# Kernel optimization log

Measured on AMD Instinct MI355X. Metric: run time of the kernel, lower is better.

Reference implementation:

```python
import jax, jax.numpy as jnp
import numpy as np

NUM_NODES = 128
BATCH = 32768
G_BASE = np.array([8.0, 8.0, 16.0, 8.0, 8.0, 4.0, 8.0, 8.0, 4.0, 4.0, 4.0, 8.0], dtype=np.float32)
T_BASE = np.array([0.02, 0.02, 0.16, 0.28], dtype=np.float32)


def setup_inputs() -> dict:
    key = jax.random.key(0)
    k1, k2, k3, k4, k5, k6 = jax.random.split(key, 6)
    x = jax.random.normal(k1, (BATCH, NUM_NODES * 8), dtype=jnp.float32)
    t = jnp.zeros((), dtype=jnp.float32)
    node_connectivity = jax.random.normal(k2, (NUM_NODES, NUM_NODES), dtype=jnp.float32) * 0.1
    # per-node gain/time-constant params (init values + small perturbation so grads are generic)
    G = jnp.asarray(G_BASE)[None, :] * (1.0 + 0.05 * jax.random.normal(k3, (NUM_NODES, 12), dtype=jnp.float32))
    T = jnp.asarray(T_BASE)[None, :] * (1.0 + 0.05 * jax.random.normal(k4, (NUM_NODES, 4), dtype=jnp.float32))
    adaptation = jnp.ones((NUM_NODES,), dtype=jnp.float32) + 0.1 * jax.random.normal(k5, (NUM_NODES,), dtype=jnp.float32)
    R = jnp.ones((NUM_NODES,), dtype=jnp.float32) + 0.1 * jax.random.normal(k6, (NUM_NODES,), dtype=jnp.float32)
    return {"t": t, "x": x, "node_connectivity": node_connectivity, "G": G, "T": T,
            "adaptation": adaptation, "R": R}


def reference(t, x, node_connectivity, G, T, adaptation, R):
    # x: [B, N*8] state; activation = sigmoid branch of FlexibleCMC
    B = x.shape[0]
    N = node_connectivity.shape[0]
    x = jnp.clip(x, -100.0, 100.0)
    xs = x.reshape(B, N, 8)  # [B, N, 8]
    # S = sigmoid(R*x) - sigmoid(0)  (sigmoid activation branch)
    S = jax.nn.sigmoid(R[None, :, None] * xs) - 0.5  # [B, N, 8]
    # message passing: mean activity of each node, weighted by connectivity (no self-loop)
    m = xs.mean(axis=-1)  # [B, N]
    C = node_connectivity * (1.0 - jnp.eye(N, dtype=node_connectivity.dtype))
    node_input = jnp.einsum('bj,ij->bi', m, C)  # [B, N]
    scale = jax.nn.sigmoid(adaptation) * 0.1  # [N]

    g = lambda k: G[:, k]  # [N], broadcasts against [B, N]
    u1 = -g(0) * S[..., 0] - g(2) * S[..., 4] - g(1) * S[..., 2] + node_input
    f1 = scale * (u1 - 2.0 * xs[..., 1] - xs[..., 0] / T[:, 0]) / T[:, 0]
    u3 = g(7) * S[..., 0] - g(6) * S[..., 2] - g(11) * S[..., 4] + node_input
    f3 = scale * (u3 - 2.0 * xs[..., 3] - xs[..., 2] / T[:, 1]) / T[:, 1]
    u5 = g(4) * S[..., 0] + g(5) * S[..., 6] - g(3) * S[..., 4] + g(10) * S[..., 2] + node_input
    f5 = scale * (u5 - 2.0 * xs[..., 5] - xs[..., 4] / T[:, 2]) / T[:, 2]
    u7 = -g(9) * S[..., 6] - g(8) * S[..., 4] + node_input
    f7 = scale * (u7 - 2.0 * xs[..., 7] - xs[..., 6] / T[:, 3]) / T[:, 3]
    f0 = scale * xs[..., 1]
    f2 = scale * xs[..., 3]
    f4 = scale * xs[..., 5]
    f6 = scale * xs[..., 7]
    f = jnp.stack([f0, f1, f2, f3, f4, f5, f6, f7], axis=-1)  # [B, N, 8]
    return f.reshape(B, N * 8)
```

## Files before the change

kernel.cpp:

```cpp
#include <hip/hip_runtime.h>

#define NNODES 128
#define BATCH  32768
#define BLOCK  256
#define ROWS_PER_CHUNK 8
#define NCHUNKS (BATCH / ROWS_PER_CHUNK)
#define GRID   1024

__device__ __forceinline__ float sigmoidf_(float z) {
    return 1.0f / (1.0f + __expf(-z));
}

__device__ __forceinline__ float clipf_(float v) {
    return fminf(fmaxf(v, -100.0f), 100.0f);
}

__device__ __forceinline__ unsigned short bf16_(float f) {
    unsigned u = __float_as_uint(f);
    return (unsigned short)((u + 0x8000u) >> 16);
}

__device__ __forceinline__ void node_update(const float* xs8, float ni,
                                            const float* gi, const float* invTi,
                                            float sci, float Ri, float* f8) {
    float S0 = sigmoidf_(Ri * xs8[0]) - 0.5f;
    float S2 = sigmoidf_(Ri * xs8[2]) - 0.5f;
    float S4 = sigmoidf_(Ri * xs8[4]) - 0.5f;
    float S6 = sigmoidf_(Ri * xs8[6]) - 0.5f;
    float u1 = ni - gi[0] * S0 - gi[1] * S2 - gi[2]  * S4;
    float u3 = ni + gi[7] * S0 - gi[6] * S2 - gi[11] * S4;
    float u5 = ni + gi[4] * S0 + gi[10] * S2 - gi[3] * S4 + gi[5] * S6;
    float u7 = ni - gi[8] * S4 - gi[9] * S6;
    f8[0] = sci * xs8[1];
    f8[1] = sci * (u1 - 2.0f * xs8[1] - xs8[0] * invTi[0]) * invTi[0];
    f8[2] = sci * xs8[3];
    f8[3] = sci * (u3 - 2.0f * xs8[3] - xs8[2] * invTi[1]) * invTi[1];
    f8[4] = sci * xs8[5];
    f8[5] = sci * (u5 - 2.0f * xs8[5] - xs8[4] * invTi[2]) * invTi[2];
    f8[6] = sci * xs8[7];
    f8[7] = sci * (u7 - 2.0f * xs8[7] - xs8[6] * invTi[3]) * invTi[3];
}

__global__ __launch_bounds__(BLOCK, 2)
void cmc_kernel(const float* __restrict__ x,
                const float* __restrict__ C,
                const float* __restrict__ G,
                const float* __restrict__ T,
                const float* __restrict__ adap,
                const float* __restrict__ R,
                float* __restrict__ out)
{
    __shared__ uint4 ct4[32 * 64];
    __shared__ float m_lds[4][2][NNODES];

    const int tid  = threadIdx.x;
    const int lane = tid & 63;
    const int w    = tid >> 6;
    const int nA   = 2 * lane;

    {
        const int j0 = (tid & 31) * 4;
        const int j4 = j0 >> 2;
        const int tb = tid >> 5;
        #pragma unroll
        for (int it = 0; it < 4; ++it) {
            const int i0 = (tb + it * 8) * 4;
            float4 row[4];
            #pragma unroll
            for (int r = 0; r < 4; ++r)
                row[r] = *reinterpret_cast<const float4*>(C + (size_t)(i0 + r) * NNODES + j0);
            unsigned short t[4][4];
            #pragma unroll
            for (int r = 0; r < 4; ++r) {
                #pragma unroll
                for (int jj = 0; jj < 4; ++jj)
                    t[r][jj] = (i0 + r == j0 + jj) ? (unsigned short)0
                                                   : bf16_((&row[r].x)[jj]);
            }
            uint4 rec0, rec1;
            rec0.x = (unsigned)t[0][0] | ((unsigned)t[0][1] << 16);
            rec0.y = (unsigned)t[0][2] | ((unsigned)t[0][3] << 16);
            rec0.z = (unsigned)t[1][0] | ((unsigned)t[1][1] << 16);
            rec0.w = (unsigned)t[1][2] | ((unsigned)t[1][3] << 16);
            rec1.x = (unsigned)t[2][0] | ((unsigned)t[2][1] << 16);
            rec1.y = (unsigned)t[2][2] | ((unsigned)t[2][3] << 16);
            rec1.z = (unsigned)t[3][0] | ((unsigned)t[3][1] << 16);
            rec1.w = (unsigned)t[3][2] | ((unsigned)t[3][3] << 16);
            const int p0 = i0 >> 1;
            ct4[j4 * 64 + (p0 ^ j4)]       = rec0;
            ct4[j4 * 64 + ((p0 + 1) ^ j4)] = rec1;
        }
    }

    float g[2][12], invT[2][4], sc[2], Rr[2];
    #pragma unroll
    for (int i = 0; i < 2; ++i) {
        int n = nA + i;
        #pragma unroll
        for (int k = 0; k < 12; ++k) g[i][k] = G[n * 12 + k];
        #pragma unroll
        for (int k = 0; k < 4; ++k) invT[i][k] = 1.0f / T[n * 4 + k];
        sc[i] = 0.1f * sigmoidf_(adap[n]);
        Rr[i] = R[n];
    }

    __syncthreads();

    for (int chunk = blockIdx.x; chunk < NCHUNKS; chunk += GRID) {
        const int r0 = chunk * ROWS_PER_CHUNK + 2 * w;

        float xv[2][16];
        {
            const float4* p0 = reinterpret_cast<const float4*>(x + (size_t)r0 * 1024 + lane * 16);
            const float4* p1 = reinterpret_cast<const float4*>(x + (size_t)(r0 + 1) * 1024 + lane * 16);
            #pragma unroll
            for (int q = 0; q < 4; ++q) {
                float4 v = p0[q];
                xv[0][q * 4 + 0] = clipf_(v.x); xv[0][q * 4 + 1] = clipf_(v.y);
                xv[0][q * 4 + 2] = clipf_(v.z); xv[0][q * 4 + 3] = clipf_(v.w);
            }
            #pragma unroll
            for (int q = 0; q < 4; ++q) {
                float4 v = p1[q];
                xv[1][q * 4 + 0] = clipf_(v.x); xv[1][q * 4 + 1] = clipf_(v.y);
                xv[1][q * 4 + 2] = clipf_(v.z); xv[1][q * 4 + 3] = clipf_(v.w);
            }
        }

        #pragma unroll
        for (int rr = 0; rr < 2; ++rr) {
            float s0 = 0.0f, s1 = 0.0f;
            #pragma unroll
            for (int k = 0; k < 8; ++k) { s0 += xv[rr][k]; s1 += xv[rr][8 + k]; }
            float2 mv = make_float2(s0 * 0.125f, s1 * 0.125f);
            *reinterpret_cast<float2*>(&m_lds[w][rr][nA]) = mv;
        }

        float acc00 = 0.f, acc01 = 0.f, acc10 = 0.f, acc11 = 0.f;
        #pragma unroll 4
        for (int j4 = 0; j4 < 32; ++j4) {
            float4 mA = *reinterpret_cast<const float4*>(&m_lds[w][0][j4 * 4]);
            float4 mB = *reinterpret_cast<const float4*>(&m_lds[w][1][j4 * 4]);
            uint4 cu = ct4[j4 * 64 + (lane ^ j4)];
            float ce0 = __uint_as_float(cu.x << 16);
            float ce1 = __uint_as_float(cu.x & 0xffff0000u);
            float ce2 = __uint_as_float(cu.y << 16);
            float ce3 = __uint_as_float(cu.y & 0xffff0000u);
            float co0 = __uint_as_float(cu.z << 16);
            float co1 = __uint_as_float(cu.z & 0xffff0000u);
            float co2 = __uint_as_float(cu.w << 16);
            float co3 = __uint_as_float(cu.w & 0xffff0000u);
            acc00 = fmaf(mA.x, ce0, acc00); acc00 = fmaf(mA.y, ce1, acc00);
            acc00 = fmaf(mA.z, ce2, acc00); acc00 = fmaf(mA.w, ce3, acc00);
            acc01 = fmaf(mA.x, co0, acc01); acc01 = fmaf(mA.y, co1, acc01);
            acc01 = fmaf(mA.z, co2, acc01); acc01 = fmaf(mA.w, co3, acc01);
            acc10 = fmaf(mB.x, ce0, acc10); acc10 = fmaf(mB.y, ce1, acc10);
            acc10 = fmaf(mB.z, ce2, acc10); acc10 = fmaf(mB.w, ce3, acc10);
            acc11 = fmaf(mB.x, co0, acc11); acc11 = fmaf(mB.y, co1, acc11);
            acc11 = fmaf(mB.z, co2, acc11); acc11 = fmaf(mB.w, co3, acc11);
        }

        {
            float* o0 = out + (size_t)r0 * 1024 + lane * 16;
            float* o1 = out + (size_t)(r0 + 1) * 1024 + lane * 16;
            float f8[8];
            node_update(&xv[0][0], acc00, g[0], invT[0], sc[0], Rr[0], f8);
            *reinterpret_cast<float4*>(o0)      = make_float4(f8[0], f8[1], f8[2], f8[3]);
            *reinterpret_cast<float4*>(o0 + 4)  = make_float4(f8[4], f8[5], f8[6], f8[7]);
            node_update(&xv[0][8], acc01, g[1], invT[1], sc[1], Rr[1], f8);
            *reinterpret_cast<float4*>(o0 + 8)  = make_float4(f8[0], f8[1], f8[2], f8[3]);
            *reinterpret_cast<float4*>(o0 + 12) = make_float4(f8[4], f8[5], f8[6], f8[7]);
            node_update(&xv[1][0], acc10, g[0], invT[0], sc[0], Rr[0], f8);
            *reinterpret_cast<float4*>(o1)      = make_float4(f8[0], f8[1], f8[2], f8[3]);
            *reinterpret_cast<float4*>(o1 + 4)  = make_float4(f8[4], f8[5], f8[6], f8[7]);
            node_update(&xv[1][8], acc11, g[1], invT[1], sc[1], Rr[1], f8);
            *reinterpret_cast<float4*>(o1 + 8)  = make_float4(f8[0], f8[1], f8[2], f8[3]);
            *reinterpret_cast<float4*>(o1 + 12) = make_float4(f8[4], f8[5], f8[6], f8[7]);
        }
    }
}

extern "C" void kernel_launch(void* const* d_in, const int* in_sizes, int n_in,
                              void* d_out, int out_size, void* d_ws, size_t ws_size,
                              hipStream_t stream) {
    const float* x    = (const float*)d_in[1];
    const float* C    = (const float*)d_in[2];
    const float* G    = (const float*)d_in[3];
    const float* T    = (const float*)d_in[4];
    const float* adap = (const float*)d_in[5];
    const float* R    = (const float*)d_in[6];
    float* out        = (float*)d_out;

    hipLaunchKernelGGL(cmc_kernel, dim3(GRID), dim3(BLOCK), 0, stream,
                       x, C, G, T, adap, R, out);
}
```

Baseline: 64.62 us.

## Software-pipeline chunk loads with double-buffered registers and unrolled four-chunk schedule

Replaces the grid-stride loop with a fully unrolled schedule of four chunks per block, prefetching the next chunk's x rows into a second register buffer while the current chunk is processed. The per-wave mean buffer in LDS is doubled so the two in-flight chunks do not alias. The launch bound's minimum-blocks hint is dropped, which lets the compiler use more registers for the extra buffers at the cost of possible lower occupancy. The schedule hardcodes exactly four chunks per block, so it relies on NCHUNKS being 4*GRID.

```diff
diff --git a/kernel.cpp b/kernel.cpp
--- a/kernel.cpp
+++ b/kernel.cpp
@@ -41,7 +41,77 @@
     f8[7] = sci * (u7 - 2.0f * xs8[7] - xs8[6] * invTi[3]) * invTi[3];
 }
 
-__global__ __launch_bounds__(BLOCK, 2)
+__device__ __forceinline__ void load_rows(const float* __restrict__ x, int r0, int lane,
+                                          float4 (&buf)[8]) {
+    const float4* p0 = reinterpret_cast<const float4*>(x + (size_t)r0 * 1024 + lane * 16);
+    const float4* p1 = reinterpret_cast<const float4*>(x + (size_t)(r0 + 1) * 1024 + lane * 16);
+    buf[0] = p0[0]; buf[1] = p0[1]; buf[2] = p0[2]; buf[3] = p0[3];
+    buf[4] = p1[0]; buf[5] = p1[1]; buf[6] = p1[2]; buf[7] = p1[3];
+}
+
+__device__ __forceinline__ void process_chunk(float4 (&buf)[8], int r0, int lane,
+                                              const float (&g)[2][12], const float (&invT)[2][4],
+                                              const float (&sc)[2], const float (&Rr)[2],
+                                              const uint4* __restrict__ ct4s,
+                                              float* __restrict__ m0, float* __restrict__ m1,
+                                              float* __restrict__ out) {
+    float* bf = &buf[0].x;
+    #pragma unroll
+    for (int k = 0; k < 32; ++k) bf[k] = clipf_(bf[k]);
+
+    {
+        float s00 = 0.f, s01 = 0.f, s10 = 0.f, s11 = 0.f;
+        #pragma unroll
+        for (int k = 0; k < 8; ++k) {
+            s00 += bf[k]; s01 += bf[8 + k]; s10 += bf[16 + k]; s11 += bf[24 + k];
+        }
+        const int nA = 2 * lane;
+        *reinterpret_cast<float2*>(&m0[nA]) = make_float2(s00 * 0.125f, s01 * 0.125f);
+        *reinterpret_cast<float2*>(&m1[nA]) = make_float2(s10 * 0.125f, s11 * 0.125f);
+    }
+
+    float acc00 = 0.f, acc01 = 0.f, acc10 = 0.f, acc11 = 0.f;
+    #pragma unroll 4
+    for (int j4 = 0; j4 < 32; ++j4) {
+        float4 mA = *reinterpret_cast<const float4*>(&m0[j4 * 4]);
+        float4 mB = *reinterpret_cast<const float4*>(&m1[j4 * 4]);
+        uint4 cu = ct4s[j4 * 64 + (lane ^ j4)];
+        float ce0 = __uint_as_float(cu.x << 16);
+        float ce1 = __uint_as_float(cu.x & 0xffff0000u);
+        float ce2 = __uint_as_float(cu.y << 16);
+        float ce3 = __uint_as_float(cu.y & 0xffff0000u);
+        float co0 = __uint_as_float(cu.z << 16);
+        float co1 = __uint_as_float(cu.z & 0xffff0000u);
+        float co2 = __uint_as_float(cu.w << 16);
+        float co3 = __uint_as_float(cu.w & 0xffff0000u);
+        acc00 = fmaf(mA.x, ce0, acc00); acc00 = fmaf(mA.y, ce1, acc00);
+        acc00 = fmaf(mA.z, ce2, acc00); acc00 = fmaf(mA.w, ce3, acc00);
+        acc01 = fmaf(mA.x, co0, acc01); acc01 = fmaf(mA.y, co1, acc01);
+        acc01 = fmaf(mA.z, co2, acc01); acc01 = fmaf(mA.w, co3, acc01);
+        acc10 = fmaf(mB.x, ce0, acc10); acc10 = fmaf(mB.y, ce1, acc10);
+        acc10 = fmaf(mB.z, ce2, acc10); acc10 = fmaf(mB.w, ce3, acc10);
+        acc11 = fmaf(mB.x, co0, acc11); acc11 = fmaf(mB.y, co1, acc11);
+        acc11 = fmaf(mB.z, co2, acc11); acc11 = fmaf(mB.w, co3, acc11);
+    }
+
+    float* o0 = out + (size_t)r0 * 1024 + lane * 16;
+    float* o1 = o0 + 1024;
+    float f8[8];
+    node_update(&bf[0],  acc00, g[0], invT[0], sc[0], Rr[0], f8);
+    *reinterpret_cast<float4*>(o0)      = make_float4(f8[0], f8[1], f8[2], f8[3]);
+    *reinterpret_cast<float4*>(o0 + 4)  = make_float4(f8[4], f8[5], f8[6], f8[7]);
+    node_update(&bf[8],  acc01, g[1], invT[1], sc[1], Rr[1], f8);
+    *reinterpret_cast<float4*>(o0 + 8)  = make_float4(f8[0], f8[1], f8[2], f8[3]);
+    *reinterpret_cast<float4*>(o0 + 12) = make_float4(f8[4], f8[5], f8[6], f8[7]);
+    node_update(&bf[16], acc10, g[0], invT[0], sc[0], Rr[0], f8);
+    *reinterpret_cast<float4*>(o1)      = make_float4(f8[0], f8[1], f8[2], f8[3]);
+    *reinterpret_cast<float4*>(o1 + 4)  = make_float4(f8[4], f8[5], f8[6], f8[7]);
+    node_update(&bf[24], acc11, g[1], invT[1], sc[1], Rr[1], f8);
+    *reinterpret_cast<float4*>(o1 + 8)  = make_float4(f8[0], f8[1], f8[2], f8[3]);
+    *reinterpret_cast<float4*>(o1 + 12) = make_float4(f8[4], f8[5], f8[6], f8[7]);
+}
+
+__global__ __launch_bounds__(BLOCK)
 void cmc_kernel(const float* __restrict__ x,
                 const float* __restrict__ C,
                 const float* __restrict__ G,
@@ -51,7 +121,7 @@
                 float* __restrict__ out)
 {
     __shared__ uint4 ct4[32 * 64];
-    __shared__ float m_lds[4][2][NNODES];
+    __shared__ float m_lds[4][2][2][NNODES];
 
     const int tid  = threadIdx.x;
     const int lane = tid & 63;
@@ -106,78 +176,26 @@
 
     __syncthreads();
 
-    for (int chunk = blockIdx.x; chunk < NCHUNKS; chunk += GRID) {
-        const int r0 = chunk * ROWS_PER_CHUNK + 2 * w;
-
-        float xv[2][16];
-        {
-            const float4* p0 = reinterpret_cast<const float4*>(x + (size_t)r0 * 1024 + lane * 16);
-            const float4* p1 = reinterpret_cast<const float4*>(x + (size_t)(r0 + 1) * 1024 + lane * 16);
-            #pragma unroll
-            for (int q = 0; q < 4; ++q) {
-                float4 v = p0[q];
-                xv[0][q * 4 + 0] = clipf_(v.x); xv[0][q * 4 + 1] = clipf_(v.y);
-                xv[0][q * 4 + 2] = clipf_(v.z); xv[0][q * 4 + 3] = clipf_(v.w);
-            }
-            #pragma unroll
-            for (int q = 0; q < 4; ++q) {
-                float4 v = p1[q];
-                xv[1][q * 4 + 0] = clipf_(v.x); xv[1][q * 4 + 1] = clipf_(v.y);
-                xv[1][q * 4 + 2] = clipf_(v.z); xv[1][q * 4 + 3] = clipf_(v.w);
-            }
-        }
-
-        #pragma unroll
-        for (int rr = 0; rr < 2; ++rr) {
-            float s0 = 0.0f, s1 = 0.0f;
-            #pragma unroll
-            for (int k = 0; k < 8; ++k) { s0 += xv[rr][k]; s1 += xv[rr][8 + k]; }
-            float2 mv = make_float2(s0 * 0.125f, s1 * 0.125f);
-            *reinterpret_cast<float2*>(&m_lds[w][rr][nA]) = mv;
-        }
-
-        float acc00 = 0.f, acc01 = 0.f, acc10 = 0.f, acc11 = 0.f;
-        #pragma unroll 4
-        for (int j4 = 0; j4 < 32; ++j4) {
-            float4 mA = *reinterpret_cast<const float4*>(&m_lds[w][0][j4 * 4]);
-            float4 mB = *reinterpret_cast<const float4*>(&m_lds[w][1][j4 * 4]);
-            uint4 cu = ct4[j4 * 64 + (lane ^ j4)];
-            float ce0 = __uint_as_float(cu.x << 16);
-            float ce1 = __uint_as_float(cu.x & 0xffff0000u);
-            float ce2 = __uint_as_float(cu.y << 16);
-            float ce3 = __uint_as_float(cu.y & 0xffff0000u);
-            float co0 = __uint_as_float(cu.z << 16);
-            float co1 = __uint_as_float(cu.z & 0xffff0000u);
-            float co2 = __uint_as_float(cu.w << 16);
-            float co3 = __uint_as_float(cu.w & 0xffff0000u);
-            acc00 = fmaf(mA.x, ce0, acc00); acc00 = fmaf(mA.y, ce1, acc00);
-            acc00 = fmaf(mA.z, ce2, acc00); acc00 = fmaf(mA.w, ce3, acc00);
-            acc01 = fmaf(mA.x, co0, acc01); acc01 = fmaf(mA.y, co1, acc01);
-            acc01 = fmaf(mA.z, co2, acc01); acc01 = fmaf(mA.w, co3, acc01);
-            acc10 = fmaf(mB.x, ce0, acc10); acc10 = fmaf(mB.y, ce1, acc10);
-            acc10 = fmaf(mB.z, ce2, acc10); acc10 = fmaf(mB.w, ce3, acc10);
-            acc11 = fmaf(mB.x, co0, acc11); acc11 = fmaf(mB.y, co1, acc11);
-            acc11 = fmaf(mB.z, co2, acc11); acc11 = fmaf(mB.w, co3, acc11);
-        }
-
-        {
-            float* o0 = out + (size_t)r0 * 1024 + lane * 16;
-            float* o1 = out + (size_t)(r0 + 1) * 1024 + lane * 16;
-            float f8[8];
-            node_update(&xv[0][0], acc00, g[0], invT[0], sc[0], Rr[0], f8);
-            *reinterpret_cast<float4*>(o0)      = make_float4(f8[0], f8[1], f8[2], f8[3]);
-            *reinterpret_cast<float4*>(o0 + 4)  = make_float4(f8[4], f8[5], f8[6], f8[7]);
-            node_update(&xv[0][8], acc01, g[1], invT[1], sc[1], Rr[1], f8);
-            *reinterpret_cast<float4*>(o0 + 8)  = make_float4(f8[0], f8[1], f8[2], f8[3]);
-            *reinterpret_cast<float4*>(o0 + 12) = make_float4(f8[4], f8[5], f8[6], f8[7]);
-            node_update(&xv[1][0], acc10, g[0], invT[0], sc[0], Rr[0], f8);
-            *reinterpret_cast<float4*>(o1)      = make_float4(f8[0], f8[1], f8[2], f8[3]);
-            *reinterpret_cast<float4*>(o1 + 4)  = make_float4(f8[4], f8[5], f8[6], f8[7]);
-            node_update(&xv[1][8], acc11, g[1], invT[1], sc[1], Rr[1], f8);
-            *reinterpret_cast<float4*>(o1 + 8)  = make_float4(f8[0], f8[1], f8[2], f8[3]);
-            *reinterpret_cast<float4*>(o1 + 12) = make_float4(f8[4], f8[5], f8[6], f8[7]);
-        }
-    }
+    const int c0 = blockIdx.x;
+    const int c1 = c0 + GRID;
+    const int c2 = c1 + GRID;
+    const int c3 = c2 + GRID;
+    const int rbase = 2 * w;
+    float* mA0 = &m_lds[w][0][0][0]; float* mA1 = &m_lds[w][0][1][0];
+    float* mB0 = &m_lds[w][1][0][0]; float* mB1 = &m_lds[w][1][1][0];
+
+    float4 bufA[8], bufB[8];
+    load_rows(x, c0 * ROWS_PER_CHUNK + rbase, lane, bufA);
+    load_rows(x, c1 * ROWS_PER_CHUNK + rbase, lane, bufB);
+
+    process_chunk(bufA, c0 * ROWS_PER_CHUNK + rbase, lane, g, invT, sc, Rr, ct4, mA0, mA1, out);
+    load_rows(x, c2 * ROWS_PER_CHUNK + rbase, lane, bufA);
+
+    process_chunk(bufB, c1 * ROWS_PER_CHUNK + rbase, lane, g, invT, sc, Rr, ct4, mB0, mB1, out);
+    load_rows(x, c3 * ROWS_PER_CHUNK + rbase, lane, bufB);
+
+    process_chunk(bufA, c2 * ROWS_PER_CHUNK + rbase, lane, g, invT, sc, Rr, ct4, mA0, mA1, out);
+    process_chunk(bufB, c3 * ROWS_PER_CHUNK + rbase, lane, g, invT, sc, Rr, ct4, mB0, mB1, out);
 }
 
 extern "C" void kernel_launch(void* const* d_in, const int* in_sizes, int n_in,
```

Result: no change. 65.67 us (+1.6%).
